# Performance work log

Hardware: AMD Instinct MI355X
Metric: run time of the kernel (lower is better)

The kernel has to match this reference:

```python
import jax, jax.numpy as jnp
import numpy as np

D_MODEL = 1024
NUM_HEADS = 16
HEAD_DIM = D_MODEL // NUM_HEADS
FF_DIM = 4096
EPS = 1e-5


def _layer_norm(x, gamma, beta):
    mu = jnp.mean(x, axis=-1, keepdims=True)
    var = jnp.var(x, axis=-1, keepdims=True)
    return (x - mu) * jax.lax.rsqrt(var + EPS) * gamma + beta


def setup_inputs() -> dict:
    key0 = jax.random.key(0)
    ks = jax.random.split(key0, 20)
    s = 0.02
    B, S = 2, 2048
    inp = {
        'value': jax.random.normal(ks[0], (B, S, D_MODEL), jnp.float32),
        'key': jax.random.normal(ks[1], (B, S, D_MODEL), jnp.float32),
        'query': jax.random.normal(ks[2], (B, S, D_MODEL), jnp.float32),
        # attention projections (stored [in, out]; y = x @ W + b)
        'wq': jax.random.normal(ks[3], (D_MODEL, D_MODEL), jnp.float32) * s,
        'bq': jnp.zeros((D_MODEL,), jnp.float32),
        'wk': jax.random.normal(ks[4], (D_MODEL, D_MODEL), jnp.float32) * s,
        'bk': jnp.zeros((D_MODEL,), jnp.float32),
        'wv': jax.random.normal(ks[5], (D_MODEL, D_MODEL), jnp.float32) * s,
        'bv': jnp.zeros((D_MODEL,), jnp.float32),
        'wo': jax.random.normal(ks[6], (D_MODEL, D_MODEL), jnp.float32) * s,
        'bo': jnp.zeros((D_MODEL,), jnp.float32),
        # layernorm 1
        'g1': jnp.ones((D_MODEL,), jnp.float32),
        'beta1': jnp.zeros((D_MODEL,), jnp.float32),
        # feed-forward
        'w1': jax.random.normal(ks[7], (D_MODEL, FF_DIM), jnp.float32) * s,
        'b1': jnp.zeros((FF_DIM,), jnp.float32),
        'w2': jax.random.normal(ks[8], (FF_DIM, D_MODEL), jnp.float32) * s,
        'b2': jnp.zeros((D_MODEL,), jnp.float32),
        # layernorm 2
        'g2': jnp.ones((D_MODEL,), jnp.float32),
        'beta2': jnp.zeros((D_MODEL,), jnp.float32),
    }
    return inp


def reference(value, key, query, wq, bq, wk, bk, wv, bv, wo, bo,
              g1, beta1, w1, b1, w2, b2, g2, beta2):
    B, S, _ = query.shape
    # QKV projections -> [B, S, H, Dh]
    Q = (query @ wq + bq).reshape(B, S, NUM_HEADS, HEAD_DIM)
    K = (key @ wk + bk).reshape(B, S, NUM_HEADS, HEAD_DIM)
    V = (value @ wv + bv).reshape(B, S, NUM_HEADS, HEAD_DIM)
    # scaled dot-product attention (full score matrix, as in source)
    energy = jnp.einsum('bqhd,bkhd->bhqk', Q, K) / jnp.sqrt(jnp.float32(HEAD_DIM))
    attn = jax.nn.softmax(energy, axis=-1)
    out = jnp.einsum('bhqk,bkhd->bqhd', attn, V).reshape(B, S, D_MODEL)
    attn_out = out @ wo + bo
    # residual + norm1 (dropout is identity in eval)
    x = _layer_norm(attn_out + query, g1, beta1)
    # feed-forward
    ff = jax.nn.relu(x @ w1 + b1) @ w2 + b2
    # residual + norm2
    return _layer_norm(ff + x, g2, beta2)
```

## Files before the change

kernel.cpp:

```cpp
#include <hip/hip_runtime.h>
#include <hip/hip_bf16.h>
#include <cstdint>
#include <math.h>

typedef __bf16 bf16_t;
typedef __attribute__((ext_vector_type(2))) __bf16 bf16x2;
typedef __attribute__((ext_vector_type(4))) __bf16 bf16x4;
typedef __attribute__((ext_vector_type(8))) __bf16 bf16x8;
typedef __attribute__((ext_vector_type(4))) float f32x4;
typedef __attribute__((ext_vector_type(16))) float f32x16;
typedef __attribute__((ext_vector_type(2))) int int2v;
typedef __attribute__((ext_vector_type(4))) int int4v;

#define B_SZ 2
#define S_SZ 2048
#define D_MODEL 1024
#define NUM_HEADS 16
#define HEAD_DIM 64
#define FF_DIM 4096
#define M_ROWS (B_SZ * S_SZ)

#define CF 0.180336880f
#define THRC 2.0f

__device__ __forceinline__ float fexp2(float x) { return __builtin_amdgcn_exp2f(x); }

__device__ __forceinline__ void gload_lds16(const void* g, void* lds) {
    __builtin_amdgcn_global_load_lds(
        (const __attribute__((address_space(1))) void*)(uintptr_t)g,
        (__attribute__((address_space(3))) void*)(uint32_t)(uintptr_t)lds,
        16, 0, 0);
}

__device__ __forceinline__ f32x4 mfma16(bf16x8 a, bf16x8 b, f32x4 c) {
    return __builtin_amdgcn_mfma_f32_16x16x32_bf16(a, b, c, 0, 0, 0);
}
__device__ __forceinline__ f32x16 mfma32(bf16x8 a, bf16x8 b, f32x16 c) {
    return __builtin_amdgcn_mfma_f32_32x32x16_bf16(a, b, c, 0, 0, 0);
}
__device__ __forceinline__ int2v plswap(int a, int b) {
    return __builtin_amdgcn_permlane32_swap(a, b, false, false);
}
__device__ __forceinline__ int packbf(float a, float b) {
    bf16x2 t; t[0] = (bf16_t)a; t[1] = (bf16_t)b;
    return __builtin_bit_cast(int, t);
}

__device__ __forceinline__ int xcd_swz(int lin, int nwg) {
    return (lin & 7) * (nwg >> 3) + (lin >> 3);
}

__global__ __launch_bounds__(256) void cast3_f32_bf16(const float* __restrict__ in0,
                                                      const float* __restrict__ in1,
                                                      const float* __restrict__ in2,
                                                      bf16_t* __restrict__ out0,
                                                      bf16_t* __restrict__ out1,
                                                      bf16_t* __restrict__ out2) {
    int which = blockIdx.x >> 12;
    int blk = blockIdx.x & 4095;
    const float* in = which == 0 ? in0 : which == 1 ? in1 : in2;
    bf16_t* out = which == 0 ? out0 : which == 1 ? out1 : out2;
    size_t i = ((size_t)blk * 256 + threadIdx.x) * 4;
    float4 v = *(const float4*)(in + i);
    bf16x4 o;
    o[0] = (bf16_t)v.x; o[1] = (bf16_t)v.y; o[2] = (bf16_t)v.z; o[3] = (bf16_t)v.w;
    *(bf16x4*)(out + i) = o;
}

__global__ __launch_bounds__(256) void transpose_cast_w4(const float* __restrict__ W0,
                                                         const float* __restrict__ W1,
                                                         const float* __restrict__ W2,
                                                         const float* __restrict__ W3,
                                                         bf16_t* __restrict__ T0,
                                                         bf16_t* __restrict__ T1,
                                                         bf16_t* __restrict__ T2,
                                                         bf16_t* __restrict__ T3) {
    __shared__ float t[32][33];
    const int K = 1024, N = 1024;
    const float* W = blockIdx.z == 0 ? W0 : blockIdx.z == 1 ? W1 : blockIdx.z == 2 ? W2 : W3;
    bf16_t* WT = blockIdx.z == 0 ? T0 : blockIdx.z == 1 ? T1 : blockIdx.z == 2 ? T2 : T3;
    int tid = threadIdx.x;
    int rr = tid >> 3, cc = (tid & 7) * 4;
    int k0 = blockIdx.x * 32, n0 = blockIdx.y * 32;
    float4 v = *(const float4*)(W + (size_t)(k0 + rr) * N + n0 + cc);
    t[rr][cc + 0] = v.x; t[rr][cc + 1] = v.y; t[rr][cc + 2] = v.z; t[rr][cc + 3] = v.w;
    __syncthreads();
    bf16x4 o;
    o[0] = (bf16_t)t[cc + 0][rr]; o[1] = (bf16_t)t[cc + 1][rr];
    o[2] = (bf16_t)t[cc + 2][rr]; o[3] = (bf16_t)t[cc + 3][rr];
    *(bf16x4*)(WT + (size_t)(n0 + rr) * K + k0 + cc) = o;
}

__global__ __launch_bounds__(256) void transpose_cast_w(const float* __restrict__ W,
                                                        bf16_t* __restrict__ WT,
                                                        int K, int N) {
    __shared__ float t[32][33];
    int tid = threadIdx.x;
    int rr = tid >> 3, cc = (tid & 7) * 4;
    int k0 = blockIdx.x * 32, n0 = blockIdx.y * 32;
    float4 v = *(const float4*)(W + (size_t)(k0 + rr) * N + n0 + cc);
    t[rr][cc + 0] = v.x; t[rr][cc + 1] = v.y; t[rr][cc + 2] = v.z; t[rr][cc + 3] = v.w;
    __syncthreads();
    bf16x4 o;
    o[0] = (bf16_t)t[cc + 0][rr]; o[1] = (bf16_t)t[cc + 1][rr];
    o[2] = (bf16_t)t[cc + 2][rr]; o[3] = (bf16_t)t[cc + 3][rr];
    *(bf16x4*)(WT + (size_t)(n0 + rr) * K + k0 + cc) = o;
}

__global__ __launch_bounds__(256) void transpose_v(const bf16_t* __restrict__ Vp,
                                                   bf16_t* __restrict__ VT) {
    __shared__ bf16_t t[32][34];
    int tid = threadIdx.x;
    int rr = tid >> 3, cc = (tid & 7) * 4;
    int bh = blockIdx.z;
    int b = bh >> 4, h = bh & 15;
    int s0 = blockIdx.x * 32, d0 = blockIdx.y * 32;
    bf16x4 v = *(const bf16x4*)(Vp + ((size_t)(b * S_SZ + s0 + rr)) * D_MODEL + h * HEAD_DIM + d0 + cc);
    t[rr][cc + 0] = v[0]; t[rr][cc + 1] = v[1]; t[rr][cc + 2] = v[2]; t[rr][cc + 3] = v[3];
    __syncthreads();
    bf16x4 o;
    o[0] = t[cc + 0][rr]; o[1] = t[cc + 1][rr]; o[2] = t[cc + 2][rr]; o[3] = t[cc + 3][rr];
    *(bf16x4*)(VT + ((size_t)(bh * HEAD_DIM + d0 + rr)) * S_SZ + s0 + cc) = o;
}

template<int NJT, bool RELU, bool OUT_BF16, bool OUT_F32>
__device__ __forceinline__ void gemm8p_core(const bf16_t* __restrict__ Ag, int lda,
                                            const bf16_t* __restrict__ Bg, int ldb,
                                            const float* __restrict__ bias, bool useBias,
                                            float* __restrict__ Cf,
                                            bf16_t* __restrict__ Cb,
                                            int N, int Klen, int m0, int n0,
                                            bf16_t* sA, bf16_t* sB) {
    constexpr int BELE = 8192 * NJT;
    constexpr int NBQ = 2 * NJT;
    const int tid = threadIdx.x;
    const int lane = tid & 63, w = tid >> 6;
    const int l31 = lane & 31, hi = lane >> 5;
    const int wm = (w >> 2) * 128;
    const int wn = (w & 3) * (32 * NJT);
    const int rs7 = l31 & 7;

    const int scol = ((tid & 7) ^ ((tid >> 3) & 7)) * 8;
    const bf16_t* aSrc = Ag + (size_t)(m0 + (tid >> 3)) * lda + scol;
    const bf16_t* bSrc = Bg + (size_t)(n0 + (tid >> 3)) * ldb + scol;

    f32x16 acc[4][NJT];
#pragma unroll
    for (int it = 0; it < 4; it++)
#pragma unroll
        for (int jt = 0; jt < NJT; jt++)
#pragma unroll
            for (int e = 0; e < 16; e++) acc[it][jt][e] = 0.f;

    auto stA = [&](int buf, int q, int k0) {
        gload_lds16(aSrc + (size_t)(q * 64) * lda + k0, sA + buf * 16384 + q * 4096 + tid * 8);
    };
    auto stB = [&](int buf, int q, int k0) {
        gload_lds16(bSrc + (size_t)(q * 64) * ldb + k0, sB + buf * BELE + q * 4096 + tid * 8);
    };

    bf16x8 a[4], b[NJT];
    auto RD = [&](int buf, int ks) {
        const bf16_t* bA = sA + buf * 16384;
        const bf16_t* bB = sB + buf * BELE;
        const int cs = ((((ks << 1) | hi)) ^ rs7) << 3;
#pragma unroll
        for (int it = 0; it < 4; it++)
            a[it] = *(const bf16x8*)(bA + (wm + it * 32 + l31) * 64 + cs);
#pragma unroll
        for (int jt = 0; jt < NJT; jt++)
            b[jt] = *(const bf16x8*)(bB + (wn + jt * 32 + l31) * 64 + cs);
    };
    auto MM = [&]() {
        __builtin_amdgcn_s_setprio(1);
#pragma unroll
        for (int it = 0; it < 4; it++)
#pragma unroll
            for (int jt = 0; jt < NJT; jt++)
                acc[it][jt] = mfma32(a[it], b[jt], acc[it][jt]);
        __builtin_amdgcn_s_setprio(0);
    };

#define LGKM0() do { asm volatile("s_waitcnt lgkmcnt(0)" ::: "memory"); \
                     __builtin_amdgcn_sched_barrier(0); } while (0)

    const int nk = Klen >> 6;
#pragma unroll
    for (int q = 0; q < 4; q++) stA(0, q, 0);
#pragma unroll
    for (int q = 0; q < NBQ; q++) stB(0, q, 0);
    asm volatile("s_waitcnt vmcnt(0)" ::: "memory");
    __builtin_amdgcn_s_barrier();

    for (int t = 0; t < nk; ++t) {
        const int buf = t & 1, nb = buf ^ 1;
        const int kn = (t + 1) << 6;
        const bool hn = (t + 1 < nk);
        RD(buf, 0);
        if (hn) { stA(nb, 0, kn); stA(nb, 1, kn); stA(nb, 2, kn); }
        LGKM0();
        MM();
        RD(buf, 1);
        if (hn) { stA(nb, 3, kn); stB(nb, 0, kn); if (NBQ > 1) stB(nb, 1, kn); }
        LGKM0();
        MM();
        RD(buf, 2);
        if (hn && NBQ > 2) { stB(nb, 2, kn); stB(nb, 3, kn); }
        LGKM0();
        MM();
        RD(buf, 3);
        LGKM0();
        MM();
        asm volatile("s_waitcnt vmcnt(0)" ::: "memory");
        __builtin_amdgcn_s_barrier();
    }
#undef LGKM0

#pragma unroll
    for (int it = 0; it < 4; it++) {
#pragma unroll
        for (int jt = 0; jt < NJT; jt++) {
            const int n = n0 + wn + jt * 32 + l31;
            const float bv = useBias ? bias[n] : 0.f;
#pragma unroll
            for (int e = 0; e < 16; e++) {
                const int mrow = m0 + wm + it * 32 + (e & 3) + ((e >> 2) << 3) + hi * 4;
                float val = acc[it][jt][e] + bv;
                if (RELU) val = fmaxf(val, 0.f);
                if (OUT_F32) Cf[(size_t)mrow * N + n] = val;
                if (OUT_BF16) Cb[(size_t)mrow * N + n] = (bf16_t)val;
            }
        }
    }
}

template<int NJT, bool RELU, bool OUT_BF16, bool OUT_F32>
__global__ __launch_bounds__(512, 1) void gemm8p(const bf16_t* __restrict__ A, int lda,
                                                 const bf16_t* __restrict__ Bt, int ldb,
                                                 const float* __restrict__ bias,
                                                 float* __restrict__ Cf0,
                                                 float* __restrict__ Cf1,
                                                 bf16_t* __restrict__ Cb,
                                                 int N, int Klen) {
    __shared__ bf16_t sA[2 * 16384];
    __shared__ bf16_t sB[2 * 8192 * NJT];
    const int lin = blockIdx.x + gridDim.x * (blockIdx.y + gridDim.y * blockIdx.z);
    const int nwg = gridDim.x * gridDim.y * gridDim.z;
    const int sz = xcd_swz(lin, nwg);
    const int bx = sz % gridDim.x;
    const int rest = sz / gridDim.x;
    const int by = rest % gridDim.y;
    const int bz = rest / gridDim.y;
    const int koff = bz * Klen;
    gemm8p_core<NJT, RELU, OUT_BF16, OUT_F32>(A + koff, lda, Bt + koff, ldb,
                                              bias, bz == 0,
                                              bz ? Cf1 : Cf0, Cb, N, Klen,
                                              bx * 256, by * (128 * NJT), sA, sB);
}

__global__ __launch_bounds__(512, 1) void gemm_qkv8p(const bf16_t* __restrict__ A0,
                                                     const bf16_t* __restrict__ A1,
                                                     const bf16_t* __restrict__ A2,
                                                     const bf16_t* __restrict__ B0,
                                                     const bf16_t* __restrict__ B1,
                                                     const bf16_t* __restrict__ B2,
                                                     const float* __restrict__ b0,
                                                     const float* __restrict__ b1,
                                                     const float* __restrict__ b2,
                                                     bf16_t* __restrict__ C0,
                                                     bf16_t* __restrict__ C1,
                                                     bf16_t* __restrict__ C2) {
    __shared__ bf16_t sA[2 * 16384];
    __shared__ bf16_t sB[2 * 16384];
    const int lin = blockIdx.x + gridDim.x * (blockIdx.y + gridDim.y * blockIdx.z);
    const int nwg = gridDim.x * gridDim.y * gridDim.z;
    const int sz = xcd_swz(lin, nwg);
    const int bx = sz % gridDim.x;
    const int rest = sz / gridDim.x;
    const int by = rest % gridDim.y;
    const int bz = rest / gridDim.y;
    const bf16_t* A = bz == 0 ? A0 : bz == 1 ? A1 : A2;
    const bf16_t* Bt = bz == 0 ? B0 : bz == 1 ? B1 : B2;
    const float* bias = bz == 0 ? b0 : bz == 1 ? b1 : b2;
    bf16_t* C = bz == 0 ? C0 : bz == 1 ? C1 : C2;
    gemm8p_core<2, false, true, false>(A, 1024, Bt, 1024, bias, true,
                                       nullptr, C, 1024, 1024, bx * 256, by * 256, sA, sB);
}

__device__ __forceinline__ void flash_tile(
    const char* kt, const char* vt, int l31, int hi,
    const bf16x8 (&bq)[4],
    f32x16& o0, f32x16& o1, float& mC, float& l_run)
{
    bf16x8 ak[4];
#pragma unroll
    for (int kb = 0; kb < 4; kb++)
        ak[kb] = *(const bf16x8*)(kt + l31 * 128 + (((kb << 1) | hi) ^ (l31 & 7)) * 16);
    bf16x8 av[4];
#pragma unroll
    for (int db = 0; db < 2; db++)
#pragma unroll
        for (int kb = 0; kb < 2; kb++)
            av[db * 2 + kb] = *(const bf16x8*)(vt + (db * 32 + l31) * 64 + ((((kb << 1) | hi)) ^ ((l31 >> 1) & 3)) * 16);

    f32x16 s;
#pragma unroll
    for (int e = 0; e < 16; e++) s[e] = 0.f;
#pragma unroll
    for (int kb = 0; kb < 4; kb++) s = mfma32(ak[kb], bq[kb], s);

    float ma = fmaxf(fmaxf(s[0], s[1]), fmaxf(s[2], s[3]));
    float mb = fmaxf(fmaxf(s[4], s[5]), fmaxf(s[6], s[7]));
    float mc = fmaxf(fmaxf(s[8], s[9]), fmaxf(s[10], s[11]));
    float md = fmaxf(fmaxf(s[12], s[13]), fmaxf(s[14], s[15]));
    float pmaxC = fmaxf(fmaxf(ma, mb), fmaxf(mc, md)) * CF;

    if (!__all(pmaxC <= mC + THRC)) {
        int2v pr = plswap(__float_as_int(pmaxC), __float_as_int(pmaxC));
        float rowmaxC = fmaxf(__int_as_float(pr[0]), __int_as_float(pr[1]));
        float mnewC = fmaxf(mC, rowmaxC);
        float alpha = fexp2(mC - mnewC);
        mC = mnewC;
        l_run *= alpha;
#pragma unroll
        for (int e = 0; e < 16; e++) { o0[e] *= alpha; o1[e] *= alpha; }
    }

#pragma unroll
    for (int e = 0; e < 16; e++) s[e] = fexp2(__builtin_fmaf(s[e], CF, -mC));
    float t0 = (s[0] + s[1]) + (s[2] + s[3]);
    float t1 = (s[4] + s[5]) + (s[6] + s[7]);
    float t2 = (s[8] + s[9]) + (s[10] + s[11]);
    float t3 = (s[12] + s[13]) + (s[14] + s[15]);
    l_run += (t0 + t1) + (t2 + t3);

#pragma unroll
    for (int kb2 = 0; kb2 < 2; kb2++) {
        const int bse = kb2 * 8;
        int W0 = packbf(s[bse + 0], s[bse + 1]);
        int W1 = packbf(s[bse + 2], s[bse + 3]);
        int W2 = packbf(s[bse + 4], s[bse + 5]);
        int W3 = packbf(s[bse + 6], s[bse + 7]);
        int2v r02 = plswap(W0, W2);
        int2v r13 = plswap(W1, W3);
        int4v fw; fw[0] = r02[0]; fw[1] = r13[0]; fw[2] = r02[1]; fw[3] = r13[1];
        bf16x8 pf = __builtin_bit_cast(bf16x8, fw);
        o0 = mfma32(av[kb2], pf, o0);
        o1 = mfma32(av[2 + kb2], pf, o1);
    }
}

__global__ __launch_bounds__(256) void flash_attn(const bf16_t* __restrict__ Qp,
                                                  const bf16_t* __restrict__ Kp,
                                                  const bf16_t* __restrict__ VT,
                                                  bf16_t* __restrict__ Oa) {
    __shared__ alignas(16) char lds[2][2][8192];
    const int tid = threadIdx.x;
    const int lane = tid & 63;
    const int wave = tid >> 6;
    const int half = wave >> 1;
    const int qt = wave & 1;
    const int l31 = lane & 31, hi = lane >> 5;

    const int lin = blockIdx.x + (blockIdx.y << 5) + (blockIdx.z << 9);
    const int swz = (lin & 7) * 128 + (lin >> 3);
    const int qb = swz & 31;
    const int h = (swz >> 5) & 15;
    const int b = swz >> 9;

    const int q0 = qb * 64 + qt * 32;

    const bf16_t* Qb = Qp + (size_t)b * S_SZ * D_MODEL + h * HEAD_DIM;
    const bf16_t* Kb = Kp + (size_t)b * S_SZ * D_MODEL + h * HEAD_DIM;
    const bf16_t* Vb = VT + ((size_t)(b * NUM_HEADS + h) * HEAD_DIM) * S_SZ;

    const int sh = wave & 1;
    const int skvbase = sh * (S_SZ / 2);
    const bool kRole = wave < 2;

    const bf16_t* src_run;
    size_t inner_stride;
    size_t tile_stride;
    char* dst0;
    char* dst1;
    if (kRole) {
        src_run = Kb + (size_t)(skvbase + (lane >> 3)) * D_MODEL + ((lane & 7) ^ (lane >> 3)) * 8;
        inner_stride = (size_t)8 * D_MODEL;
        tile_stride = (size_t)32 * D_MODEL;
        dst0 = &lds[0][sh][0] + lane * 16;
        dst1 = &lds[1][sh][0] + lane * 16;
    } else {
        src_run = Vb + (size_t)(lane >> 2) * S_SZ + skvbase + ((lane & 3) ^ ((lane >> 3) & 3)) * 8;
        inner_stride = (size_t)16 * S_SZ;
        tile_stride = 32;
        dst0 = &lds[0][sh][4096] + lane * 16;
        dst1 = &lds[1][sh][4096] + lane * 16;
    }

    bf16x8 bq[4];
#pragma unroll
    for (int kb = 0; kb < 4; kb++)
        bq[kb] = *(const bf16x8*)(Qb + (size_t)(q0 + l31) * D_MODEL + kb * 16 + hi * 8);

    f32x16 o0, o1;
#pragma unroll
    for (int e = 0; e < 16; e++) { o0[e] = 0.f; o1[e] = 0.f; }
    float mC = -1e30f, l_run = 0.f;

    const char* kt0 = &lds[0][half][0];
    const char* vt0 = &lds[0][half][4096];
    const char* kt1 = &lds[1][half][0];
    const char* vt1 = &lds[1][half][4096];

#pragma unroll
    for (int ii = 0; ii < 4; ii++)
        gload_lds16(src_run + ii * inner_stride, dst0 + ii * 1024);
    src_run += tile_stride;
    __syncthreads();

    for (int t = 0; t < 32; t += 2) {
#pragma unroll
        for (int ii = 0; ii < 4; ii++)
            gload_lds16(src_run + ii * inner_stride, dst1 + ii * 1024);
        src_run += tile_stride;
        flash_tile(kt0, vt0, l31, hi, bq, o0, o1, mC, l_run);
        __syncthreads();

        if (t + 2 < 32) {
#pragma unroll
            for (int ii = 0; ii < 4; ii++)
                gload_lds16(src_run + ii * inner_stride, dst0 + ii * 1024);
            src_run += tile_stride;
        }
        flash_tile(kt1, vt1, l31, hi, bq, o0, o1, mC, l_run);
        __syncthreads();
    }

    int2v lp = plswap(__float_as_int(l_run), __float_as_int(l_run));
    l_run = __int_as_float(lp[0]) + __int_as_float(lp[1]);

    float (*obuf)[2][64] = (float (*)[2][64])(&lds[0][0][0]);
    float (*mrg)[64][2] = (float (*)[64][2])(&lds[0][0][0] + 16384);
    if (half == 1) {
        mrg[qt][lane][0] = mC;
        mrg[qt][lane][1] = l_run;
#pragma unroll
        for (int e = 0; e < 16; e++) {
            obuf[e][qt][lane] = o0[e];
            obuf[16 + e][qt][lane] = o1[e];
        }
    }
    __syncthreads();
    if (half == 0) {
        const float m2C = mrg[qt][lane][0], l2 = mrg[qt][lane][1];
        const float mm = fmaxf(mC, m2C);
        const float e1 = fexp2(mC - mm);
        const float e2 = fexp2(m2C - mm);
        const float linv = 1.f / (l_run * e1 + l2 * e2);
        bf16_t* Orow = Oa + ((size_t)b * S_SZ + q0 + l31) * D_MODEL + h * HEAD_DIM;
#pragma unroll
        for (int db = 0; db < 2; db++) {
#pragma unroll
            for (int rq = 0; rq < 4; rq++) {
                bf16x4 st;
#pragma unroll
                for (int i = 0; i < 4; i++) {
                    const int e = rq * 4 + i;
                    const float own = db ? o1[e] : o0[e];
                    const float oth = obuf[db * 16 + e][qt][lane];
                    st[i] = (bf16_t)((own * e1 + oth * e2) * linv);
                }
                *(bf16x4*)(Orow + db * 32 + rq * 8 + hi * 4) = st;
            }
        }
    }
}

__global__ __launch_bounds__(256) void ln_fused(const float* __restrict__ A,
                                                const float* __restrict__ A2,
                                                const float* __restrict__ R,
                                                const float* __restrict__ gamma,
                                                const float* __restrict__ beta,
                                                float* __restrict__ Xf,
                                                bf16_t* __restrict__ Xb) {
    __shared__ float red[8];
    int row = blockIdx.x, tid = threadIdx.x;
    size_t base = (size_t)row * D_MODEL + tid * 4;
    float4 a = *(const float4*)(A + base);
    float4 rv = *(const float4*)(R + base);
    float v0 = a.x + rv.x, v1 = a.y + rv.y, v2 = a.z + rv.z, v3 = a.w + rv.w;
    if (A2) {
        float4 a2 = *(const float4*)(A2 + base);
        v0 += a2.x; v1 += a2.y; v2 += a2.z; v3 += a2.w;
    }
    float s = v0 + v1 + v2 + v3;
    float q = v0 * v0 + v1 * v1 + v2 * v2 + v3 * v3;
#pragma unroll
    for (int off = 32; off; off >>= 1) { s += __shfl_down(s, off); q += __shfl_down(q, off); }
    if ((tid & 63) == 0) { red[tid >> 6] = s; red[4 + (tid >> 6)] = q; }
    __syncthreads();
    s = red[0] + red[1] + red[2] + red[3];
    q = red[4] + red[5] + red[6] + red[7];
    float mean = s * (1.f / D_MODEL);
    float var = q * (1.f / D_MODEL) - mean * mean;
    float rstd = rsqrtf(var + 1e-5f);
    float4 gm = *(const float4*)(gamma + tid * 4);
    float4 bt = *(const float4*)(beta + tid * 4);
    float y0 = (v0 - mean) * rstd * gm.x + bt.x;
    float y1 = (v1 - mean) * rstd * gm.y + bt.y;
    float y2 = (v2 - mean) * rstd * gm.z + bt.z;
    float y3 = (v3 - mean) * rstd * gm.w + bt.w;
    float4 yo; yo.x = y0; yo.y = y1; yo.z = y2; yo.w = y3;
    *(float4*)(Xf + base) = yo;
    if (Xb) {
        bf16x4 ob; ob[0] = (bf16_t)y0; ob[1] = (bf16_t)y1; ob[2] = (bf16_t)y2; ob[3] = (bf16_t)y3;
        *(bf16x4*)(Xb + base) = ob;
    }
}

extern "C" void kernel_launch(void* const* d_in, const int* in_sizes, int n_in,
                              void* d_out, int out_size, void* d_ws, size_t ws_size,
                              hipStream_t stream) {
    const float* value = (const float*)d_in[0];
    const float* key   = (const float*)d_in[1];
    const float* query = (const float*)d_in[2];
    const float* wq = (const float*)d_in[3];
    const float* bq = (const float*)d_in[4];
    const float* wk = (const float*)d_in[5];
    const float* bk = (const float*)d_in[6];
    const float* wv = (const float*)d_in[7];
    const float* bv = (const float*)d_in[8];
    const float* wo = (const float*)d_in[9];
    const float* bo = (const float*)d_in[10];
    const float* g1 = (const float*)d_in[11];
    const float* beta1 = (const float*)d_in[12];
    const float* w1 = (const float*)d_in[13];
    const float* b1 = (const float*)d_in[14];
    const float* w2 = (const float*)d_in[15];
    const float* b2 = (const float*)d_in[16];
    const float* g2 = (const float*)d_in[17];
    const float* beta2 = (const float*)d_in[18];
    (void)in_sizes; (void)n_in; (void)out_size; (void)ws_size;

    const size_t MB = 1ull << 20;
    char* ws = (char*)d_ws;
    bf16_t* wqT = (bf16_t*)(ws + 0 * MB);
    bf16_t* wkT = (bf16_t*)(ws + 2 * MB);
    bf16_t* wvT = (bf16_t*)(ws + 4 * MB);
    bf16_t* woT = (bf16_t*)(ws + 6 * MB);
    bf16_t* w1T = (bf16_t*)(ws + 8 * MB);
    bf16_t* w2T = (bf16_t*)(ws + 16 * MB);
    bf16_t* q_bf = (bf16_t*)(ws + 24 * MB);
    bf16_t* k_bf = (bf16_t*)(ws + 32 * MB);
    bf16_t* v_bf = (bf16_t*)(ws + 40 * MB);
    bf16_t* Qp  = (bf16_t*)(ws + 48 * MB);
    bf16_t* Kp  = (bf16_t*)(ws + 56 * MB);
    bf16_t* Vp  = (bf16_t*)(ws + 64 * MB);
    bf16_t* VT  = (bf16_t*)(ws + 72 * MB);
    bf16_t* attn = (bf16_t*)(ws + 24 * MB);
    float*  woP0 = (float*)(ws + 32 * MB);
    float*  woP1 = (float*)(ws + 48 * MB);
    float*  x_f = (float*)(ws + 64 * MB);
    bf16_t* x_b = (bf16_t*)(ws + 24 * MB);
    bf16_t* h_b = (bf16_t*)(ws + 32 * MB);
    float*  ffP0 = (float*)(ws + 80 * MB);
    float*  ffP1 = (float*)(ws + 96 * MB);

    dim3 blk(256);
    dim3 blk512(512);

    cast3_f32_bf16<<<12288, blk, 0, stream>>>(query, key, value, q_bf, k_bf, v_bf);
    transpose_cast_w4<<<dim3(32, 32, 4), blk, 0, stream>>>(wq, wk, wv, wo, wqT, wkT, wvT, woT);
    transpose_cast_w<<<dim3(32, 128), blk, 0, stream>>>(w1, w1T, 1024, 4096);
    transpose_cast_w<<<dim3(128, 32), blk, 0, stream>>>(w2, w2T, 4096, 1024);

    gemm_qkv8p<<<dim3(16, 4, 3), blk512, 0, stream>>>(q_bf, k_bf, v_bf, wqT, wkT, wvT,
                                                      bq, bk, bv, Qp, Kp, Vp);

    transpose_v<<<dim3(64, 2, 32), blk, 0, stream>>>(Vp, VT);

    flash_attn<<<dim3(32, 16, 2), blk, 0, stream>>>(Qp, Kp, VT, attn);

    gemm8p<1, false, false, true><<<dim3(16, 8, 2), blk512, 0, stream>>>(attn, 1024, woT, 1024, bo, woP0, woP1, nullptr, D_MODEL, 512);

    ln_fused<<<4096, blk, 0, stream>>>(woP0, woP1, query, g1, beta1, x_f, x_b);

    gemm8p<2, true, true, false><<<dim3(16, 16, 1), blk512, 0, stream>>>(x_b, 1024, w1T, 1024, b1, nullptr, nullptr, h_b, FF_DIM, 1024);

    gemm8p<1, false, false, true><<<dim3(16, 8, 2), blk512, 0, stream>>>(h_b, 4096, w2T, 4096, b2, ffP0, ffP1, nullptr, D_MODEL, 2048);

    ln_fused<<<4096, blk, 0, stream>>>(ffP0, ffP1, x_f, g2, beta2, (float*)d_out, nullptr);
}
```

Measured before the change: 240.8 us.

## Fuse fp32-to-bf16 activation cast into QKV projection GEMM A-tile loads

Drops the separate cast kernel for query/key/value and has the QKV GEMM load fp32 activations into registers, convert them to bf16 and write them into swizzled LDS, while B still uses direct global-to-LDS loads. This removes one launch plus a full write and re-read of three bf16 activation buffers. In exchange the GEMM reads twice the A bytes as fp32, holds more registers for staged A data, and loses the async LDS path for A, which could weaken its software pipeline.

```diff
diff --git a/kernel.cpp b/kernel.cpp
--- a/kernel.cpp
+++ b/kernel.cpp
@@ -48,23 +48,6 @@
 
 __device__ __forceinline__ int xcd_swz(int lin, int nwg) {
     return (lin & 7) * (nwg >> 3) + (lin >> 3);
-}
-
-__global__ __launch_bounds__(256) void cast3_f32_bf16(const float* __restrict__ in0,
-                                                      const float* __restrict__ in1,
-                                                      const float* __restrict__ in2,
-                                                      bf16_t* __restrict__ out0,
-                                                      bf16_t* __restrict__ out1,
-                                                      bf16_t* __restrict__ out2) {
-    int which = blockIdx.x >> 12;
-    int blk = blockIdx.x & 4095;
-    const float* in = which == 0 ? in0 : which == 1 ? in1 : in2;
-    bf16_t* out = which == 0 ? out0 : which == 1 ? out1 : out2;
-    size_t i = ((size_t)blk * 256 + threadIdx.x) * 4;
-    float4 v = *(const float4*)(in + i);
-    bf16x4 o;
-    o[0] = (bf16_t)v.x; o[1] = (bf16_t)v.y; o[2] = (bf16_t)v.z; o[3] = (bf16_t)v.w;
-    *(bf16x4*)(out + i) = o;
 }
 
 __global__ __launch_bounds__(256) void transpose_cast_w4(const float* __restrict__ W0,
@@ -258,9 +241,9 @@
                                               bx * 256, by * (128 * NJT), sA, sB);
 }
 
-__global__ __launch_bounds__(512, 1) void gemm_qkv8p(const bf16_t* __restrict__ A0,
-                                                     const bf16_t* __restrict__ A1,
-                                                     const bf16_t* __restrict__ A2,
+__global__ __launch_bounds__(512, 1) void gemm_qkv8p(const float* __restrict__ A0,
+                                                     const float* __restrict__ A1,
+                                                     const float* __restrict__ A2,
                                                      const bf16_t* __restrict__ B0,
                                                      const bf16_t* __restrict__ B1,
                                                      const bf16_t* __restrict__ B2,
@@ -279,12 +262,127 @@
     const int rest = sz / gridDim.x;
     const int by = rest % gridDim.y;
     const int bz = rest / gridDim.y;
-    const bf16_t* A = bz == 0 ? A0 : bz == 1 ? A1 : A2;
+    const float* Af = bz == 0 ? A0 : bz == 1 ? A1 : A2;
     const bf16_t* Bt = bz == 0 ? B0 : bz == 1 ? B1 : B2;
     const float* bias = bz == 0 ? b0 : bz == 1 ? b1 : b2;
     bf16_t* C = bz == 0 ? C0 : bz == 1 ? C1 : C2;
-    gemm8p_core<2, false, true, false>(A, 1024, Bt, 1024, bias, true,
-                                       nullptr, C, 1024, 1024, bx * 256, by * 256, sA, sB);
+    const int m0 = bx * 256, n0 = by * 256;
+    const int N = 1024, lda = 1024, ldb = 1024, Klen = 1024;
+
+    const int tid = threadIdx.x;
+    const int lane = tid & 63, w = tid >> 6;
+    const int l31 = lane & 31, hi = lane >> 5;
+    const int wm = (w >> 2) * 128;
+    const int wn = (w & 3) * 64;
+    const int rs7 = l31 & 7;
+
+    const int scolE = ((tid & 7) ^ ((tid >> 3) & 7)) * 8;
+    const float* aSrcF = Af + (size_t)(m0 + (tid >> 3)) * lda + scolE;
+    const bf16_t* bSrc = Bt + (size_t)(n0 + (tid >> 3)) * ldb + scolE;
+
+    f32x16 acc[4][2];
+#pragma unroll
+    for (int it = 0; it < 4; it++)
+#pragma unroll
+        for (int jt = 0; jt < 2; jt++)
+#pragma unroll
+            for (int e = 0; e < 16; e++) acc[it][jt][e] = 0.f;
+
+    float4 fA[4][2];
+    auto ldA = [&](int k0) {
+#pragma unroll
+        for (int q = 0; q < 4; q++) {
+            const float* s = aSrcF + (size_t)(q * 64) * lda + k0;
+            fA[q][0] = *(const float4*)(s);
+            fA[q][1] = *(const float4*)(s + 4);
+        }
+    };
+    auto wrA = [&](int buf) {
+#pragma unroll
+        for (int q = 0; q < 4; q++) {
+            bf16x8 v;
+            v[0] = (bf16_t)fA[q][0].x; v[1] = (bf16_t)fA[q][0].y;
+            v[2] = (bf16_t)fA[q][0].z; v[3] = (bf16_t)fA[q][0].w;
+            v[4] = (bf16_t)fA[q][1].x; v[5] = (bf16_t)fA[q][1].y;
+            v[6] = (bf16_t)fA[q][1].z; v[7] = (bf16_t)fA[q][1].w;
+            *(bf16x8*)(sA + buf * 16384 + q * 4096 + tid * 8) = v;
+        }
+    };
+    auto stB = [&](int buf, int q, int k0) {
+        gload_lds16(bSrc + (size_t)(q * 64) * ldb + k0, sB + buf * 16384 + q * 4096 + tid * 8);
+    };
+
+    bf16x8 a[4], b[2];
+    auto RD = [&](int buf, int ks) {
+        const bf16_t* bA = sA + buf * 16384;
+        const bf16_t* bB = sB + buf * 16384;
+        const int cs = ((((ks << 1) | hi)) ^ rs7) << 3;
+#pragma unroll
+        for (int it = 0; it < 4; it++)
+            a[it] = *(const bf16x8*)(bA + (wm + it * 32 + l31) * 64 + cs);
+#pragma unroll
+        for (int jt = 0; jt < 2; jt++)
+            b[jt] = *(const bf16x8*)(bB + (wn + jt * 32 + l31) * 64 + cs);
+    };
+    auto MM = [&]() {
+        __builtin_amdgcn_s_setprio(1);
+#pragma unroll
+        for (int it = 0; it < 4; it++)
+#pragma unroll
+            for (int jt = 0; jt < 2; jt++)
+                acc[it][jt] = mfma32(a[it], b[jt], acc[it][jt]);
+        __builtin_amdgcn_s_setprio(0);
+    };
+
+#define LGKM0() do { asm volatile("s_waitcnt lgkmcnt(0)" ::: "memory"); \
+                     __builtin_amdgcn_sched_barrier(0); } while (0)
+
+    const int nk = Klen >> 6;
+    ldA(0);
+#pragma unroll
+    for (int q = 0; q < 4; q++) stB(0, q, 0);
+    wrA(0);
+    asm volatile("s_waitcnt vmcnt(0) lgkmcnt(0)" ::: "memory");
+    __builtin_amdgcn_s_barrier();
+
+    for (int t = 0; t < nk; ++t) {
+        const int buf = t & 1, nb = buf ^ 1;
+        const int kn = (t + 1) << 6;
+        const bool hn = (t + 1 < nk);
+        RD(buf, 0);
+        if (hn) { ldA(kn); stB(nb, 0, kn); }
+        LGKM0();
+        MM();
+        RD(buf, 1);
+        if (hn) { stB(nb, 1, kn); stB(nb, 2, kn); }
+        LGKM0();
+        MM();
+        RD(buf, 2);
+        if (hn) stB(nb, 3, kn);
+        LGKM0();
+        MM();
+        RD(buf, 3);
+        LGKM0();
+        MM();
+        if (hn) wrA(nb);
+        asm volatile("s_waitcnt vmcnt(0) lgkmcnt(0)" ::: "memory");
+        __builtin_amdgcn_s_barrier();
+    }
+#undef LGKM0
+
+#pragma unroll
+    for (int it = 0; it < 4; it++) {
+#pragma unroll
+        for (int jt = 0; jt < 2; jt++) {
+            const int n = n0 + wn + jt * 32 + l31;
+            const float bv = bias[n];
+#pragma unroll
+            for (int e = 0; e < 16; e++) {
+                const int mrow = m0 + wm + it * 32 + (e & 3) + ((e >> 2) << 3) + hi * 4;
+                C[(size_t)mrow * N + n] = (bf16_t)(acc[it][jt][e] + bv);
+            }
+        }
+    }
 }
 
 __device__ __forceinline__ void flash_tile(
@@ -550,9 +648,6 @@
     bf16_t* woT = (bf16_t*)(ws + 6 * MB);
     bf16_t* w1T = (bf16_t*)(ws + 8 * MB);
     bf16_t* w2T = (bf16_t*)(ws + 16 * MB);
-    bf16_t* q_bf = (bf16_t*)(ws + 24 * MB);
-    bf16_t* k_bf = (bf16_t*)(ws + 32 * MB);
-    bf16_t* v_bf = (bf16_t*)(ws + 40 * MB);
     bf16_t* Qp  = (bf16_t*)(ws + 48 * MB);
     bf16_t* Kp  = (bf16_t*)(ws + 56 * MB);
     bf16_t* Vp  = (bf16_t*)(ws + 64 * MB);
@@ -569,12 +664,11 @@
     dim3 blk(256);
     dim3 blk512(512);
 
-    cast3_f32_bf16<<<12288, blk, 0, stream>>>(query, key, value, q_bf, k_bf, v_bf);
     transpose_cast_w4<<<dim3(32, 32, 4), blk, 0, stream>>>(wq, wk, wv, wo, wqT, wkT, wvT, woT);
     transpose_cast_w<<<dim3(32, 128), blk, 0, stream>>>(w1, w1T, 1024, 4096);
     transpose_cast_w<<<dim3(128, 32), blk, 0, stream>>>(w2, w2T, 4096, 1024);
 
-    gemm_qkv8p<<<dim3(16, 4, 3), blk512, 0, stream>>>(q_bf, k_bf, v_bf, wqT, wkT, wvT,
+    gemm_qkv8p<<<dim3(16, 4, 3), blk512, 0, stream>>>(query, key, value, wqT, wkT, wvT,
                                                       bq, bk, bv, Qp, Kp, Vp);
 
     transpose_v<<<dim3(64, 2, 32), blk, 0, stream>>>(Vp, VT);
```

New measurement: 241.0 us. Within noise of the previous version (+0.1%).
